# Optimization experiments

Measured on AMD Instinct MI355X. Metric: run time of the kernel, lower is better.

## Reference

```python
import jax, jax.numpy as jnp
import numpy as np

B, S, D, H = 2, 2048, 1024, 16
HD = D // H  # head dim


def approx_gelu(x):
    return x * jax.nn.sigmoid(1.702 * x)


def setup_inputs() -> dict:
    key = jax.random.key(0)
    ks = jax.random.split(key, 12)
    q = jax.random.normal(ks[0], (B, S, D), jnp.float32)
    k = jax.random.normal(ks[1], (B, S, D), jnp.float32)
    v = jax.random.normal(ks[2], (B, S, D), jnp.float32)
    mask = jnp.zeros((B, 1, S, S), jnp.float32)
    sc = 0.02
    Wq = jax.random.normal(ks[3], (H, D, HD), jnp.float32) * sc
    bq = jax.random.normal(ks[4], (H, HD), jnp.float32) * sc
    Wk = jax.random.normal(ks[5], (H, D, HD), jnp.float32) * sc
    bk = jax.random.normal(ks[6], (H, HD), jnp.float32) * sc
    Wv = jax.random.normal(ks[7], (H, D, HD), jnp.float32) * sc
    bv = jax.random.normal(ks[8], (H, HD), jnp.float32) * sc
    Wo = jax.random.normal(ks[9], (D, D), jnp.float32) * sc
    bo = jax.random.normal(ks[10], (D,), jnp.float32) * sc
    return {"q": q, "k": k, "v": v, "mask": mask, "Wq": Wq, "bq": bq,
            "Wk": Wk, "bk": bk, "Wv": Wv, "bv": bv, "Wo": Wo, "bo": bo}


def reference(q, k, v, mask, Wq, bq, Wk, bk, Wv, bv, Wo, bo):
    # Per-head Q/K/V dense (no activation on projections, matching source).
    qh = jnp.einsum('bsd,hde->bhse', q, Wq) + bq[None, :, None, :]  # [B,H,S,HD]
    kh = jnp.einsum('bsd,hde->bhse', k, Wk) + bk[None, :, None, :]
    vh = jnp.einsum('bsd,hde->bhse', v, Wv) + bv[None, :, None, :]
    scale = 1.0 / jnp.sqrt(jnp.asarray(HD, qh.dtype))
    logits = jnp.einsum('bhse,bhte->bhst', qh, kh) * scale + mask  # [B,H,S,S]
    attn = jax.nn.softmax(logits, axis=-1)
    heads = jnp.einsum('bhst,bhte->bhse', attn, vh)  # [B,H,S,HD]
    # concat heads -> [B,S,D]
    x = jnp.transpose(heads, (0, 2, 1, 3)).reshape(q.shape[0], q.shape[1], D)
    return approx_gelu(x @ Wo + bo)
```

## Files before the change

### kernel.cpp

```cpp
#include <hip/hip_runtime.h>
#include <stdint.h>


typedef __bf16 bf16x8 __attribute__((ext_vector_type(8)));
typedef __bf16 bf16x4 __attribute__((ext_vector_type(4)));
typedef float f32x4 __attribute__((ext_vector_type(4)));

static constexpr float L2E  = 1.4426950408889634f;
static constexpr float QSCL = 0.18033688011112042f;
static constexpr float GELC = -2.4554669595930157f;

__device__ __forceinline__ void async_load16(const void* g, void* l) {
    __builtin_amdgcn_global_load_lds(
        (const __attribute__((address_space(1))) unsigned int*)(uintptr_t)g,
        (__attribute__((address_space(3))) unsigned int*)(unsigned int)(uintptr_t)l,
        16, 0, 0);
}

template <int ROWS>
__device__ __forceinline__ void stage_tile(const __bf16* g, int ld, __bf16* lds, int tid) {
#pragma unroll
    for (int r = 0; r < ROWS / 32; ++r) {
        int p = r * 4096 + tid * 16;
        int row = p >> 7;
        int kbp = p & 127;
        int kbl = kbp ^ ((row & 7) << 4);
        async_load16((const char*)(g + (size_t)row * ld) + kbl,
                     (char*)lds + (p & ~1023));
    }
}

__device__ __forceinline__ bf16x8 lds_frag(const __bf16* base, int row, int kb) {
    return *(const bf16x8*)((const char*)base + (row << 7) + (kb ^ ((row & 7) << 4)));
}


__global__ __launch_bounds__(256) void cvt3_kernel(const float* __restrict__ q,
                                                   const float* __restrict__ k,
                                                   const float* __restrict__ v,
                                                   __bf16* __restrict__ qb,
                                                   __bf16* __restrict__ kb,
                                                   __bf16* __restrict__ vb) {
    int z = blockIdx.y;
    const float* src = z == 0 ? q : (z == 1 ? k : v);
    __bf16* dst = z == 0 ? qb : (z == 1 ? kb : vb);
    int i = blockIdx.x * 256 + threadIdx.x;
    f32x4 val = ((const f32x4*)src)[i];
    bf16x4 o;
    o[0] = (__bf16)val[0]; o[1] = (__bf16)val[1];
    o[2] = (__bf16)val[2]; o[3] = (__bf16)val[3];
    ((bf16x4*)dst)[i] = o;
}

__global__ __launch_bounds__(256) void pack_wqkv(const float* __restrict__ Wq,
                                                 const float* __restrict__ Wk,
                                                 const float* __restrict__ Wv,
                                                 __bf16* __restrict__ out) {
    __shared__ __bf16 T[64][72];
    int tid = threadIdx.x;
    int k0 = blockIdx.x * 64, h = blockIdx.y, z = blockIdx.z;
    const float* W = z == 0 ? Wq : (z == 1 ? Wk : Wv);
#pragma unroll
    for (int it = 0; it < 4; ++it) {
        int idx = it * 1024 + tid * 4;
        int r = idx >> 6, e = idx & 63;
        f32x4 val = *(const f32x4*)(W + ((size_t)h * 1024 + k0 + r) * 64 + e);
#pragma unroll
        for (int j = 0; j < 4; ++j) T[r][e + j] = (__bf16)val[j];
    }
    __syncthreads();
    int e2 = tid >> 2, kc = (tid & 3) * 16;
    bf16x8 o0, o1;
#pragma unroll
    for (int i = 0; i < 8; ++i) { o0[i] = T[kc + i][e2]; o1[i] = T[kc + 8 + i][e2]; }
    __bf16* dst = out + ((size_t)z << 20) + (size_t)(h * 64 + e2) * 1024 + k0 + kc;
    *(bf16x8*)dst = o0;
    *(bf16x8*)(dst + 8) = o1;
}

__global__ __launch_bounds__(256) void pack_wo(const float* __restrict__ Wo,
                                               __bf16* __restrict__ out) {
    __shared__ __bf16 T[64][72];
    int tid = threadIdx.x;
    int k0 = blockIdx.x * 64, n0 = blockIdx.y * 64;
#pragma unroll
    for (int it = 0; it < 4; ++it) {
        int idx = it * 1024 + tid * 4;
        int r = idx >> 6, e = idx & 63;
        f32x4 val = *(const f32x4*)(Wo + (size_t)(k0 + r) * 1024 + n0 + e);
#pragma unroll
        for (int j = 0; j < 4; ++j) T[r][e + j] = (__bf16)val[j];
    }
    __syncthreads();
    int e2 = tid >> 2, kc = (tid & 3) * 16;
    bf16x8 o0, o1;
#pragma unroll
    for (int i = 0; i < 8; ++i) { o0[i] = T[kc + i][e2]; o1[i] = T[kc + 8 + i][e2]; }
    __bf16* dst = out + (size_t)(n0 + e2) * 1024 + k0 + kc;
    *(bf16x8*)dst = o0;
    *(bf16x8*)(dst + 8) = o1;
}

__global__ __launch_bounds__(256) void vtrans(const __bf16* __restrict__ vh,
                                              __bf16* __restrict__ vT) {
    __shared__ __bf16 T[64][72];
    int tid = threadIdx.x;
    int s0 = blockIdx.x * 64, bh = blockIdx.y, b = bh >> 4, h = bh & 15;
#pragma unroll
    for (int it = 0; it < 2; ++it) {
        int idx = it * 2048 + tid * 8;
        int r = idx >> 6, e0 = idx & 63;
        bf16x8 val = *(const bf16x8*)(vh + ((size_t)b * 2048 + s0 + r) * 1024 + h * 64 + e0);
#pragma unroll
        for (int j = 0; j < 8; ++j) T[r][e0 + j] = val[j];
    }
    __syncthreads();
    int e = tid >> 2, sc = (tid & 3) * 16;
    bf16x8 o0, o1;
#pragma unroll
    for (int i = 0; i < 8; ++i) { o0[i] = T[sc + i][e]; o1[i] = T[sc + 8 + i][e]; }
    __bf16* dst = vT + ((size_t)bh * 64 + e) * 2048 + s0 + sc;
    *(bf16x8*)dst = o0;
    *(bf16x8*)(dst + 8) = o1;
}

__global__ __launch_bounds__(256) void gemm_qkv(
    const __bf16* __restrict__ qb, const __bf16* __restrict__ kb,
    const __bf16* __restrict__ vb, const __bf16* __restrict__ w3,
    const float* __restrict__ bq, const float* __restrict__ bk,
    const float* __restrict__ bv,
    __bf16* __restrict__ qo, __bf16* __restrict__ ko, __bf16* __restrict__ vo) {
    __shared__ __bf16 As[128 * 64];
    __shared__ __bf16 Bs[128 * 64];
    int z = blockIdx.z;
    const __bf16* A = z == 0 ? qb : (z == 1 ? kb : vb);
    const __bf16* Bt = w3 + ((size_t)z << 20);
    const float* bias = z == 0 ? bq : (z == 1 ? bk : bv);
    __bf16* dst = z == 0 ? qo : (z == 1 ? ko : vo);
    float sc = z == 0 ? QSCL : 1.0f;

    int tid = threadIdx.x;
    int w = tid >> 6, lane = tid & 63, lg = lane >> 4, lr = lane & 15;
    int wr = (w >> 1) * 64, wc = (w & 1) * 64;
    int m0 = blockIdx.y * 128, n0 = blockIdx.x * 128;
    f32x4 acc[4][4] = {};
    for (int k0 = 0; k0 < 1024; k0 += 64) {
        __syncthreads();
        stage_tile<128>(A + (size_t)m0 * 1024 + k0, 1024, As, tid);
        stage_tile<128>(Bt + (size_t)n0 * 1024 + k0, 1024, Bs, tid);
        __syncthreads();
#pragma unroll
        for (int kk = 0; kk < 2; ++kk) {
            bf16x8 af[4], bfr[4];
#pragma unroll
            for (int t = 0; t < 4; ++t) {
                af[t] = lds_frag(As, wr + t * 16 + lr, lg * 16 + kk * 64);
                bfr[t] = lds_frag(Bs, wc + t * 16 + lr, lg * 16 + kk * 64);
            }
#pragma unroll
            for (int i = 0; i < 4; ++i)
#pragma unroll
                for (int j = 0; j < 4; ++j)
                    acc[i][j] = __builtin_amdgcn_mfma_f32_16x16x32_bf16(
                        af[i], bfr[j], acc[i][j], 0, 0, 0);
        }
    }
#pragma unroll
    for (int i = 0; i < 4; ++i) {
        int mb = m0 + wr + i * 16 + lg * 4;
#pragma unroll
        for (int j = 0; j < 4; ++j) {
            int n = n0 + wc + j * 16 + lr;
            float bvv = bias[n];
#pragma unroll
            for (int r = 0; r < 4; ++r)
                dst[(size_t)(mb + r) * 1024 + n] = (__bf16)((acc[i][j][r] + bvv) * sc);
        }
    }
}

__global__ __launch_bounds__(256) void gemm_out(const __bf16* __restrict__ A,
                                                const __bf16* __restrict__ Bt,
                                                const float* __restrict__ bias,
                                                float* __restrict__ dst) {
    __shared__ __bf16 As[64 * 64];
    __shared__ __bf16 Bs[128 * 64];
    int tid = threadIdx.x;
    int w = tid >> 6, lane = tid & 63, lg = lane >> 4, lr = lane & 15;
    int wr = (w >> 1) * 32, wc = (w & 1) * 64;
    int m0 = blockIdx.y * 64, n0 = blockIdx.x * 128;
    f32x4 acc[2][4] = {};
    for (int k0 = 0; k0 < 1024; k0 += 64) {
        __syncthreads();
        stage_tile<64>(A + (size_t)m0 * 1024 + k0, 1024, As, tid);
        stage_tile<128>(Bt + (size_t)n0 * 1024 + k0, 1024, Bs, tid);
        __syncthreads();
#pragma unroll
        for (int kk = 0; kk < 2; ++kk) {
            bf16x8 af[2], bfr[4];
#pragma unroll
            for (int t = 0; t < 2; ++t)
                af[t] = lds_frag(As, wr + t * 16 + lr, lg * 16 + kk * 64);
#pragma unroll
            for (int t = 0; t < 4; ++t)
                bfr[t] = lds_frag(Bs, wc + t * 16 + lr, lg * 16 + kk * 64);
#pragma unroll
            for (int i = 0; i < 2; ++i)
#pragma unroll
                for (int j = 0; j < 4; ++j)
                    acc[i][j] = __builtin_amdgcn_mfma_f32_16x16x32_bf16(
                        af[i], bfr[j], acc[i][j], 0, 0, 0);
        }
    }
#pragma unroll
    for (int i = 0; i < 2; ++i) {
        int mb = m0 + wr + i * 16 + lg * 4;
#pragma unroll
        for (int j = 0; j < 4; ++j) {
            int n = n0 + wc + j * 16 + lr;
            float bvv = bias[n];
#pragma unroll
            for (int r = 0; r < 4; ++r) {
                float v = acc[i][j][r] + bvv;
                float g = v / (1.f + exp2f(GELC * v));
                dst[(size_t)(mb + r) * 1024 + n] = g;
            }
        }
    }
}

__global__ __launch_bounds__(256) void attn_kernel(const __bf16* __restrict__ qs,
                                                   const __bf16* __restrict__ ks,
                                                   const __bf16* __restrict__ vT,
                                                   const float* __restrict__ mask,
                                                   __bf16* __restrict__ x) {
    __shared__ __bf16 Ks[2][64 * 64];
    __shared__ __bf16 Vs[2][64 * 64];
    __shared__ __bf16 Ps[4][16 * 64];
    int tid = threadIdx.x;
    int w = tid >> 6, lane = tid & 63, lg = lane >> 4, lr = lane & 15;
    int bh = blockIdx.y, b = bh >> 4, h = bh & 15;
    int qw = blockIdx.x * 64 + w * 16;

    const __bf16* Qp = qs + ((size_t)b * 2048 + qw) * 1024 + h * 64;
    bf16x8 qf[2];
    qf[0] = *(const bf16x8*)(Qp + lr * 1024 + lg * 8);
    qf[1] = *(const bf16x8*)(Qp + lr * 1024 + 32 + lg * 8);

    const float* mrow = mask + ((size_t)b * 2048 + qw + lr) * 2048;
    const __bf16* Kb = ks + ((size_t)b * 2048) * 1024 + h * 64;
    const __bf16* Vb = vT + (size_t)bh * 64 * 2048;

    float l_acc = 0.f;
    f32x4 oacc[4] = {};

    f32x4 mk[4], mkn[4];
#pragma unroll
    for (int t = 0; t < 4; ++t) mk[t] = *(const f32x4*)(mrow + t * 16 + lg * 4);
    stage_tile<64>(Kb, 1024, Ks[0], tid);
    stage_tile<64>(Vb, 2048, Vs[0], tid);

    for (int kv0 = 0; kv0 < 2048; kv0 += 64) {
        int buf = (kv0 >> 6) & 1;
        __syncthreads();
        if (kv0 + 64 < 2048) {
            stage_tile<64>(Kb + (size_t)(kv0 + 64) * 1024, 1024, Ks[buf ^ 1], tid);
            stage_tile<64>(Vb + (kv0 + 64), 2048, Vs[buf ^ 1], tid);
#pragma unroll
            for (int t = 0; t < 4; ++t)
                mkn[t] = *(const f32x4*)(mrow + kv0 + 64 + t * 16 + lg * 4);
        }
        f32x4 T[4] = {};
        __builtin_amdgcn_s_setprio(1);
#pragma unroll
        for (int kk = 0; kk < 2; ++kk)
#pragma unroll
            for (int t = 0; t < 4; ++t) {
                bf16x8 a = lds_frag(Ks[buf], t * 16 + lr, lg * 16 + kk * 64);
                T[t] = __builtin_amdgcn_mfma_f32_16x16x32_bf16(a, qf[kk], T[t], 0, 0, 0);
            }
        __builtin_amdgcn_s_setprio(0);
#pragma unroll
        for (int t = 0; t < 4; ++t) {
            bf16x4 pk;
#pragma unroll
            for (int r = 0; r < 4; ++r) {
                float p = exp2f(fmaf(mk[t][r], L2E, T[t][r]));
                l_acc += p;
                pk[r] = (__bf16)p;
            }
            *(bf16x4*)((char*)Ps[w] + lr * 128 +
                       ((t * 32 + lg * 8) ^ ((lr & 7) << 4))) = pk;
        }
#pragma unroll
        for (int t = 0; t < 4; ++t) mk[t] = mkn[t];
        __builtin_amdgcn_s_setprio(1);
#pragma unroll
        for (int kk = 0; kk < 2; ++kk) {
            bf16x8 pf = lds_frag(Ps[w], lr, lg * 16 + kk * 64);
#pragma unroll
            for (int t = 0; t < 4; ++t) {
                bf16x8 a = lds_frag(Vs[buf], t * 16 + lr, lg * 16 + kk * 64);
                oacc[t] = __builtin_amdgcn_mfma_f32_16x16x32_bf16(a, pf, oacc[t], 0, 0, 0);
            }
        }
        __builtin_amdgcn_s_setprio(0);
    }
    l_acc += __shfl_xor(l_acc, 16, 64);
    l_acc += __shfl_xor(l_acc, 32, 64);
    float inv = 1.0f / l_acc;
    size_t base = ((size_t)b * 2048 + qw + lr) * 1024 + h * 64;
#pragma unroll
    for (int t = 0; t < 4; ++t) {
        bf16x4 o;
#pragma unroll
        for (int r = 0; r < 4; ++r) o[r] = (__bf16)(oacc[t][r] * inv);
        *(bf16x4*)(x + base + t * 16 + lg * 4) = o;
    }
}


extern "C" void kernel_launch(void* const* d_in, const int* in_sizes, int n_in,
                              void* d_out, int out_size, void* d_ws, size_t ws_size,
                              hipStream_t stream) {
    const float* q    = (const float*)d_in[0];
    const float* k    = (const float*)d_in[1];
    const float* v    = (const float*)d_in[2];
    const float* mask = (const float*)d_in[3];
    const float* Wq   = (const float*)d_in[4];
    const float* bq   = (const float*)d_in[5];
    const float* Wk   = (const float*)d_in[6];
    const float* bk   = (const float*)d_in[7];
    const float* Wv   = (const float*)d_in[8];
    const float* bv   = (const float*)d_in[9];
    const float* Wo   = (const float*)d_in[10];
    const float* bo   = (const float*)d_in[11];

    char* ws = (char*)d_ws;
    __bf16* qb  = (__bf16*)(ws + (0ull  << 20));
    __bf16* kb  = (__bf16*)(ws + (8ull  << 20));
    __bf16* vb  = (__bf16*)(ws + (16ull << 20));
    __bf16* w3  = (__bf16*)(ws + (24ull << 20));
    __bf16* wo  = (__bf16*)(ws + (30ull << 20));
    __bf16* qhp = (__bf16*)(ws + (32ull << 20));
    __bf16* khp = (__bf16*)(ws + (40ull << 20));
    __bf16* vhp = (__bf16*)(ws + (48ull << 20));
    __bf16* vTp = qb;
    __bf16* xp  = kb;

    cvt3_kernel<<<dim3(4096, 3), 256, 0, stream>>>(q, k, v, qb, kb, vb);
    pack_wqkv<<<dim3(16, 16, 3), 256, 0, stream>>>(Wq, Wk, Wv, w3);
    pack_wo<<<dim3(16, 16), 256, 0, stream>>>(Wo, wo);

    gemm_qkv<<<dim3(8, 32, 3), 256, 0, stream>>>(qb, kb, vb, w3, bq, bk, bv,
                                                 qhp, khp, vhp);
    vtrans<<<dim3(32, 32), 256, 0, stream>>>(vhp, vTp);

    attn_kernel<<<dim3(32, 32), 256, 0, stream>>>(qhp, khp, vTp, mask, xp);

    gemm_out<<<dim3(8, 64), 256, 0, stream>>>(xp, wo, bo, (float*)d_out);
}
```

Before: 175.0 us.

## Rewrite attention with 32x32 MFMA, register-resident K/V and bf16 mask

The attention kernel moves from 16x16x32 MFMAs with LDS-staged K/V tiles and an LDS round-trip for P to 32x32x16 MFMAs. K and V fragments are loaded straight from global memory into registers, and P is repacked in registers with cvt_pk and permlane32_swap instead of going through LDS. A new pre-pass converts the mask to bf16 premultiplied by log2(e), halving the mask bytes the attention loop reads. The grid is remapped so each block covers two heads with 32-row query tiles. This removes LDS traffic and barriers, but each wave now loads K/V from global or L2 without sharing across the block, and bf16 rounding of the mask reduces its precision.

```diff
diff --git a/kernel.cpp b/kernel.cpp
--- a/kernel.cpp
+++ b/kernel.cpp
@@ -5,6 +5,8 @@
 typedef __bf16 bf16x8 __attribute__((ext_vector_type(8)));
 typedef __bf16 bf16x4 __attribute__((ext_vector_type(4)));
 typedef float f32x4 __attribute__((ext_vector_type(4)));
+typedef float f32x16 __attribute__((ext_vector_type(16)));
+typedef unsigned u32x4 __attribute__((ext_vector_type(4)));
 
 static constexpr float L2E  = 1.4426950408889634f;
 static constexpr float QSCL = 0.18033688011112042f;
@@ -32,6 +34,15 @@
 
 __device__ __forceinline__ bf16x8 lds_frag(const __bf16* base, int row, int kb) {
     return *(const bf16x8*)((const char*)base + (row << 7) + (kb ^ ((row & 7) << 4)));
+}
+
+__device__ __forceinline__ unsigned cvtpk(float a, float b) {
+    unsigned d;
+    asm("v_cvt_pk_bf16_f32 %0, %1, %2" : "=v"(d) : "v"(a), "v"(b));
+    return d;
+}
+__device__ __forceinline__ void pswap(unsigned& a, unsigned& b) {
+    asm("v_permlane32_swap_b32 %0, %1" : "+v"(a), "+v"(b));
 }
 
 
@@ -52,6 +63,20 @@
     ((bf16x4*)dst)[i] = o;
 }
 
+__global__ __launch_bounds__(256) void mask_prep(const float* __restrict__ m,
+                                                 __bf16* __restrict__ mb0,
+                                                 __bf16* __restrict__ mb1) {
+    int b = blockIdx.y;
+    const f32x4* src = (const f32x4*)(m + (size_t)b * 4194304);
+    __bf16* dst = b ? mb1 : mb0;
+    int i = blockIdx.x * 256 + threadIdx.x;
+    f32x4 val = src[i];
+    bf16x4 o;
+    o[0] = (__bf16)(val[0] * L2E); o[1] = (__bf16)(val[1] * L2E);
+    o[2] = (__bf16)(val[2] * L2E); o[3] = (__bf16)(val[3] * L2E);
+    ((bf16x4*)dst)[i] = o;
+}
+
 __global__ __launch_bounds__(256) void pack_wqkv(const float* __restrict__ Wq,
                                                  const float* __restrict__ Wk,
                                                  const float* __restrict__ Wv,
@@ -229,94 +254,122 @@
     }
 }
 
-__global__ __launch_bounds__(256) void attn_kernel(const __bf16* __restrict__ qs,
-                                                   const __bf16* __restrict__ ks,
-                                                   const __bf16* __restrict__ vT,
-                                                   const float* __restrict__ mask,
-                                                   __bf16* __restrict__ x) {
-    __shared__ __bf16 Ks[2][64 * 64];
-    __shared__ __bf16 Vs[2][64 * 64];
-    __shared__ __bf16 Ps[4][16 * 64];
-    int tid = threadIdx.x;
-    int w = tid >> 6, lane = tid & 63, lg = lane >> 4, lr = lane & 15;
-    int bh = blockIdx.y, b = bh >> 4, h = bh & 15;
-    int qw = blockIdx.x * 64 + w * 16;
-
-    const __bf16* Qp = qs + ((size_t)b * 2048 + qw) * 1024 + h * 64;
-    bf16x8 qf[2];
-    qf[0] = *(const bf16x8*)(Qp + lr * 1024 + lg * 8);
-    qf[1] = *(const bf16x8*)(Qp + lr * 1024 + 32 + lg * 8);
-
-    const float* mrow = mask + ((size_t)b * 2048 + qw + lr) * 2048;
-    const __bf16* Kb = ks + ((size_t)b * 2048) * 1024 + h * 64;
-    const __bf16* Vb = vT + (size_t)bh * 64 * 2048;
-
+__global__ __launch_bounds__(256, 2) void attn_kernel(
+    const __bf16* __restrict__ qs, const __bf16* __restrict__ ks,
+    const __bf16* __restrict__ vT, const __bf16* __restrict__ mb0,
+    const __bf16* __restrict__ mb1, __bf16* __restrict__ x) {
+    int tid = threadIdx.x;
+    int w = tid >> 6, l = tid & 63;
+    int q31 = l & 31, hi = l >> 5;
+    int b = blockIdx.x >> 3;
+    int h = (blockIdx.x & 7) * 2 + (w >> 1);
+    int qw = blockIdx.y * 64 + (w & 1) * 32;
+    int bh = b * 16 + h;
+
+    const __bf16* Qp = qs + ((size_t)b * 2048 + qw + q31) * 1024 + h * 64 + hi * 8;
+    bf16x8 qf[4];
+#pragma unroll
+    for (int kk = 0; kk < 4; ++kk) qf[kk] = *(const bf16x8*)(Qp + kk * 16);
+
+    const __bf16* Kp = ks + (size_t)b * 2048 * 1024 + h * 64 + hi * 8;
+    const __bf16* Vp = vT + (size_t)bh * 64 * 2048 + hi * 8;
+    const __bf16* mrow = (b ? mb1 : mb0) + ((size_t)(qw + q31)) * 2048 + hi * 4;
+
+    bf16x8 kf[2][4];
+#pragma unroll
+    for (int mt = 0; mt < 2; ++mt)
+#pragma unroll
+        for (int kk = 0; kk < 4; ++kk)
+            kf[mt][kk] = *(const bf16x8*)(Kp + (size_t)(mt * 32 + q31) * 1024 + kk * 16);
+
+    f32x16 O[2] = {};
     float l_acc = 0.f;
-    f32x4 oacc[4] = {};
-
-    f32x4 mk[4], mkn[4];
-#pragma unroll
-    for (int t = 0; t < 4; ++t) mk[t] = *(const f32x4*)(mrow + t * 16 + lg * 4);
-    stage_tile<64>(Kb, 1024, Ks[0], tid);
-    stage_tile<64>(Vb, 2048, Vs[0], tid);
 
     for (int kv0 = 0; kv0 < 2048; kv0 += 64) {
-        int buf = (kv0 >> 6) & 1;
-        __syncthreads();
+        uint2 ml[2][4];
+#pragma unroll
+        for (int mt = 0; mt < 2; ++mt)
+#pragma unroll
+            for (int g = 0; g < 4; ++g)
+                ml[mt][g] = *(const uint2*)(mrow + kv0 + mt * 32 + g * 8);
+        bf16x8 vf[2][4];
+#pragma unroll
+        for (int mt = 0; mt < 2; ++mt)
+#pragma unroll
+            for (int kk = 0; kk < 4; ++kk)
+                vf[mt][kk] = *(const bf16x8*)(Vp + (size_t)(mt * 32 + q31) * 2048 + kv0 + kk * 16);
+
+        f32x16 T[2] = {};
+        __builtin_amdgcn_s_setprio(1);
+#pragma unroll
+        for (int kk = 0; kk < 4; ++kk)
+#pragma unroll
+            for (int mt = 0; mt < 2; ++mt)
+                T[mt] = __builtin_amdgcn_mfma_f32_32x32x16_bf16(kf[mt][kk], qf[kk], T[mt], 0, 0, 0);
+        __builtin_amdgcn_s_setprio(0);
+
         if (kv0 + 64 < 2048) {
-            stage_tile<64>(Kb + (size_t)(kv0 + 64) * 1024, 1024, Ks[buf ^ 1], tid);
-            stage_tile<64>(Vb + (kv0 + 64), 2048, Vs[buf ^ 1], tid);
-#pragma unroll
-            for (int t = 0; t < 4; ++t)
-                mkn[t] = *(const f32x4*)(mrow + kv0 + 64 + t * 16 + lg * 4);
-        }
-        f32x4 T[4] = {};
+#pragma unroll
+            for (int mt = 0; mt < 2; ++mt)
+#pragma unroll
+                for (int kk = 0; kk < 4; ++kk)
+                    kf[mt][kk] = *(const bf16x8*)(Kp + (size_t)(kv0 + 64 + mt * 32 + q31) * 1024 + kk * 16);
+        }
+
+#pragma unroll
+        for (int mt = 0; mt < 2; ++mt)
+#pragma unroll
+            for (int g = 0; g < 4; ++g) {
+                float f0 = __uint_as_float(ml[mt][g].x << 16);
+                float f1 = __uint_as_float(ml[mt][g].x & 0xffff0000u);
+                float f2 = __uint_as_float(ml[mt][g].y << 16);
+                float f3 = __uint_as_float(ml[mt][g].y & 0xffff0000u);
+                float p0 = exp2f(T[mt][4 * g + 0] + f0);
+                float p1 = exp2f(T[mt][4 * g + 1] + f1);
+                float p2 = exp2f(T[mt][4 * g + 2] + f2);
+                float p3 = exp2f(T[mt][4 * g + 3] + f3);
+                l_acc += (p0 + p1) + (p2 + p3);
+                T[mt][4 * g + 0] = p0; T[mt][4 * g + 1] = p1;
+                T[mt][4 * g + 2] = p2; T[mt][4 * g + 3] = p3;
+            }
+
+        bf16x8 pf[4];
+#pragma unroll
+        for (int kk = 0; kk < 4; ++kk) {
+            int mt = kk >> 1;
+            int gA = (2 * kk) & 3, gB = gA + 1;
+            unsigned x0 = cvtpk(T[mt][4 * gA + 0], T[mt][4 * gA + 1]);
+            unsigned x1 = cvtpk(T[mt][4 * gA + 2], T[mt][4 * gA + 3]);
+            unsigned y0 = cvtpk(T[mt][4 * gB + 0], T[mt][4 * gB + 1]);
+            unsigned y1 = cvtpk(T[mt][4 * gB + 2], T[mt][4 * gB + 3]);
+            pswap(x0, y0);
+            pswap(x1, y1);
+            u32x4 packed; packed[0] = x0; packed[1] = x1; packed[2] = y0; packed[3] = y1;
+            pf[kk] = __builtin_bit_cast(bf16x8, packed);
+        }
+
         __builtin_amdgcn_s_setprio(1);
 #pragma unroll
-        for (int kk = 0; kk < 2; ++kk)
-#pragma unroll
-            for (int t = 0; t < 4; ++t) {
-                bf16x8 a = lds_frag(Ks[buf], t * 16 + lr, lg * 16 + kk * 64);
-                T[t] = __builtin_amdgcn_mfma_f32_16x16x32_bf16(a, qf[kk], T[t], 0, 0, 0);
-            }
+        for (int kk = 0; kk < 4; ++kk)
+#pragma unroll
+            for (int mt = 0; mt < 2; ++mt)
+                O[mt] = __builtin_amdgcn_mfma_f32_32x32x16_bf16(vf[mt][kk], pf[kk], O[mt], 0, 0, 0);
         __builtin_amdgcn_s_setprio(0);
-#pragma unroll
-        for (int t = 0; t < 4; ++t) {
-            bf16x4 pk;
-#pragma unroll
-            for (int r = 0; r < 4; ++r) {
-                float p = exp2f(fmaf(mk[t][r], L2E, T[t][r]));
-                l_acc += p;
-                pk[r] = (__bf16)p;
-            }
-            *(bf16x4*)((char*)Ps[w] + lr * 128 +
-                       ((t * 32 + lg * 8) ^ ((lr & 7) << 4))) = pk;
-        }
-#pragma unroll
-        for (int t = 0; t < 4; ++t) mk[t] = mkn[t];
-        __builtin_amdgcn_s_setprio(1);
-#pragma unroll
-        for (int kk = 0; kk < 2; ++kk) {
-            bf16x8 pf = lds_frag(Ps[w], lr, lg * 16 + kk * 64);
-#pragma unroll
-            for (int t = 0; t < 4; ++t) {
-                bf16x8 a = lds_frag(Vs[buf], t * 16 + lr, lg * 16 + kk * 64);
-                oacc[t] = __builtin_amdgcn_mfma_f32_16x16x32_bf16(a, pf, oacc[t], 0, 0, 0);
-            }
-        }
-        __builtin_amdgcn_s_setprio(0);
-    }
-    l_acc += __shfl_xor(l_acc, 16, 64);
+    }
+
     l_acc += __shfl_xor(l_acc, 32, 64);
     float inv = 1.0f / l_acc;
-    size_t base = ((size_t)b * 2048 + qw + lr) * 1024 + h * 64;
-#pragma unroll
-    for (int t = 0; t < 4; ++t) {
-        bf16x4 o;
-#pragma unroll
-        for (int r = 0; r < 4; ++r) o[r] = (__bf16)(oacc[t][r] * inv);
-        *(bf16x4*)(x + base + t * 16 + lg * 4) = o;
-    }
+
+    __bf16* xp = x + ((size_t)b * 2048 + qw + q31) * 1024 + h * 64 + hi * 4;
+#pragma unroll
+    for (int mt = 0; mt < 2; ++mt)
+#pragma unroll
+        for (int g = 0; g < 4; ++g) {
+            bf16x4 o;
+#pragma unroll
+            for (int c = 0; c < 4; ++c) o[c] = (__bf16)(O[mt][4 * g + c] * inv);
+            *(bf16x4*)(xp + mt * 32 + g * 8) = o;
+        }
 }
 
 
@@ -347,6 +400,8 @@
     __bf16* vhp = (__bf16*)(ws + (48ull << 20));
     __bf16* vTp = qb;
     __bf16* xp  = kb;
+    __bf16* mb0p = vb;
+    __bf16* mb1p = vhp;
 
     cvt3_kernel<<<dim3(4096, 3), 256, 0, stream>>>(q, k, v, qb, kb, vb);
     pack_wqkv<<<dim3(16, 16, 3), 256, 0, stream>>>(Wq, Wk, Wv, w3);
@@ -355,8 +410,9 @@
     gemm_qkv<<<dim3(8, 32, 3), 256, 0, stream>>>(qb, kb, vb, w3, bq, bk, bv,
                                                  qhp, khp, vhp);
     vtrans<<<dim3(32, 32), 256, 0, stream>>>(vhp, vTp);
-
-    attn_kernel<<<dim3(32, 32), 256, 0, stream>>>(qhp, khp, vTp, mask, xp);
+    mask_prep<<<dim3(4096, 2), 256, 0, stream>>>(mask, mb0p, mb1p);
+
+    attn_kernel<<<dim3(16, 32), 256, 0, stream>>>(qhp, khp, vTp, mb0p, mb1p, xp);
 
     gemm_out<<<dim3(8, 64), 256, 0, stream>>>(xp, wo, bo, (float*)d_out);
 }
```

Measured after the change: 271.3 us. 1.55x slower.
